# Kernel tuning notes

Measured on AMD Instinct MI355X. Metric: run time of the kernel, lower is better.

## Reference

```python
import jax, jax.numpy as jnp
import numpy as np

B = 2048
LF = 64
N_DEC, N_MOV, N_CAT, N_PER, N_COM = 12, 60000, 32, 100000, 20000


def setup_inputs() -> dict:
    key = jax.random.key(0)
    ks = jax.random.split(key, 10)

    def multihot(k, n):
        return jax.random.randint(k, (B, n), 0, 2, dtype=jnp.int32)

    def weight(k, n):
        # nn.Linear(n, LF, bias=False) weight, stored transposed as [n, LF]
        return jax.random.normal(k, (n, LF), dtype=jnp.float32) * 0.02

    return {
        "decade_idxs": multihot(ks[0], N_DEC),
        "movie_idxs": multihot(ks[1], N_MOV),
        "category_idxs": multihot(ks[2], N_CAT),
        "person_idxs": multihot(ks[3], N_PER),
        "company_idxs": multihot(ks[4], N_COM),
        "W_dec": weight(ks[5], N_DEC),
        "W_mov": weight(ks[6], N_MOV),
        "W_cat": weight(ks[7], N_CAT),
        "W_per": weight(ks[8], N_PER),
        "W_com": weight(ks[9], N_COM),
    }


def _norm_rows(emb, s):
    # divide rows whose multi-hot sum s is nonzero (np.flatnonzero semantics)
    mask = s != 0
    safe = jnp.where(mask, s, jnp.ones_like(s))
    return jnp.where(mask[:, None], emb / safe[:, None], emb)


def reference(decade_idxs, movie_idxs, category_idxs, person_idxs, company_idxs,
              W_dec, W_mov, W_cat, W_per, W_com):
    d = decade_idxs.astype(jnp.float32)
    m = movie_idxs.astype(jnp.float32)
    c = category_idxs.astype(jnp.float32)
    p = person_idxs.astype(jnp.float32)
    q = company_idxs.astype(jnp.float32)

    decades = d @ W_dec            # [B, LF]
    decades = _norm_rows(decades, jnp.sum(d, axis=1))

    movies = m @ W_mov
    # BUG in original module (replicated faithfully): `decades` is normalized
    # AGAIN by the movie-row sums; `movies` is never normalized.
    decades = _norm_rows(decades, jnp.sum(m, axis=1))

    categories = _norm_rows(c @ W_cat, jnp.sum(c, axis=1))
    persons = _norm_rows(p @ W_per, jnp.sum(p, axis=1))
    companies = _norm_rows(q @ W_com, jnp.sum(q, axis=1))

    return jnp.concatenate([decades, movies, categories, persons, companies], axis=1)
```

## Files before the change

kernel.cpp:

```cpp
#include <hip/hip_runtime.h>
#include <hip/hip_bf16.h>

#define LF 64
#define NBAGS 5
#define BROWS 2048
#define OUTC 320
#define KC 2048
#define MT_BLOCK 128
#define NMT (BROWS / MT_BLOCK)
#define NCHUNKS 90

#define WS_HEAD 65536
#define ZP_OFF 49152
#define WP_BYTES 23068672ull
#define PART_OFF (WS_HEAD + WP_BYTES)
#define PART_BYTES ((size_t)NCHUNKS * BROWS * LF * 4)

typedef __attribute__((ext_vector_type(8))) short short8;
typedef __attribute__((ext_vector_type(4))) float f32x4;

typedef const __attribute__((address_space(1))) void gas_t;
typedef __attribute__((address_space(3))) void las_t;

struct BagArgs {
    const int*   A[NBAGS];
    const float* W[NBAGS];
    int K[NBAGS];
    int cstart[NBAGS + 1];
    int tstart[NBAGS + 1];
};

__device__ __forceinline__ unsigned short f2bf(float f) {
    unsigned u = __float_as_uint(f);
    u += 0x7FFFu + ((u >> 16) & 1u);
    return (unsigned short)(u >> 16);
}

__global__ __launch_bounds__(256) void pack_w(BagArgs args,
                                              unsigned short* __restrict__ Wp) {
    __shared__ unsigned short ls[4][4096];
    const int wv = threadIdx.x >> 6;
    const int c  = threadIdx.x & 63;
    const int gtile = blockIdx.x * 4 + wv;

    int bag = 0;
#pragma unroll
    for (int b = 1; b < NBAGS; ++b)
        if (gtile >= args.tstart[b]) bag = b;
    const int lt = gtile - args.tstart[bag];
    const float* __restrict__ W = args.W[bag];
    const int K = args.K[bag];

    unsigned short* L = ls[wv];
#pragma unroll 8
    for (int k = 0; k < 64; ++k) {
        const int gk = lt * 64 + k;
        float v = (gk < K) ? W[(size_t)gk * LF + c] : 0.f;
        const int block = ((k >> 3) & 1) * 4 + (k >> 4);
        L[(block * LF + c) * 8 + (k & 7)] = f2bf(v);
    }
    __syncthreads();
    unsigned short* dst = Wp + ((size_t)gtile << 12);
#pragma unroll
    for (int j = 0; j < 8; ++j)
        *(short8*)(dst + c * 8 + j * 512) = *(const short8*)(L + c * 8 + j * 512);
}

__global__ __launch_bounds__(256) void bag_gemm(BagArgs args,
                                                const unsigned short* __restrict__ Wp,
                                                const int* __restrict__ zp,
                                                float* __restrict__ part,
                                                int* __restrict__ sums)
{
    __shared__ char lds[2][40960];

    const int tid  = threadIdx.x;
    const int wave = tid >> 6;
    const int lane = tid & 63;
    const int fr   = lane & 15;
    const int kg   = lane >> 4;

    const int g  = blockIdx.x >> 4;
    const int mt = blockIdx.x & 15;

    int bag = 1;
#pragma unroll
    for (int b = 2; b < NBAGS; ++b)
        if (g >= args.cstart[b]) bag = b;
    const int chunk  = g - args.cstart[bag];
    const int K      = args.K[bag];
    const int kc0    = chunk * KC;
    const int kend   = min(kc0 + KC, K);
    const int nsuper = (kend - kc0 + 63) >> 6;
    const int tile0  = args.tstart[bag] + chunk * (KC / 64);

    const int row0 = mt * MT_BLOCK + wave * 32;
    const int* __restrict__ Abase = args.A[bag];

    auto stage = [&](int ss, int bufi) {
        char* dA = &lds[bufi][0] + wave * 8192;
#pragma unroll
        for (int i = 0; i < 8; ++i) {
            const int rs = i & 1, j = i >> 1;
            const int col = kc0 + ss * 64 + kg * 16 + j * 4;
            const int row = row0 + rs * 16 + fr;
            const int* src = Abase + (size_t)row * K + col;
            if (col >= kend) src = zp;
            __builtin_amdgcn_global_load_lds((gas_t*)src, (las_t*)(dA + i * 1024),
                                             16, 0, 0);
        }
        const char* sB = (const char*)Wp + ((size_t)(tile0 + ss) << 13)
                         + wave * 2048 + lane * 16;
        char* dB = &lds[bufi][32768] + wave * 2048;
        __builtin_amdgcn_global_load_lds((gas_t*)sB, (las_t*)dB, 16, 0, 0);
        __builtin_amdgcn_global_load_lds((gas_t*)(sB + 1024), (las_t*)(dB + 1024),
                                         16, 0, 0);
    };

    f32x4 acc0[4], acc1[4];
#pragma unroll
    for (int i = 0; i < 4; ++i) {
        acc0[i] = (f32x4){0.f, 0.f, 0.f, 0.f};
        acc1[i] = (f32x4){0.f, 0.f, 0.f, 0.f};
    }
    int ps0 = 0, ps1 = 0;

    stage(0, 0);
    if (nsuper > 1) stage(1, 1);

    for (int ss = 0; ss < nsuper; ++ss) {
        const int cur = ss & 1;
        if (ss + 1 < nsuper) asm volatile("s_waitcnt vmcnt(10)" ::: "memory");
        else                 asm volatile("s_waitcnt vmcnt(0)"  ::: "memory");
        __builtin_amdgcn_sched_barrier(0);
        __builtin_amdgcn_s_barrier();

        const char* Ab = &lds[cur][0]     + wave * 8192 + kg * 256 + fr * 16;
        const char* Bb = &lds[cur][32768] + kg * 1024 + fr * 16;

        short8 fa[2][2];
#pragma unroll
        for (int m = 0; m < 2; ++m)
#pragma unroll
            for (int rs = 0; rs < 2; ++rs) {
                int4 lo = *(const int4*)(Ab + (size_t)(4 * m + rs) * 1024);
                int4 hi = *(const int4*)(Ab + (size_t)(4 * m + 2 + rs) * 1024);
                const int s = lo.x + lo.y + lo.z + lo.w + hi.x + hi.y + hi.z + hi.w;
                if (rs == 0) ps0 += s; else ps1 += s;
                const unsigned q0 = (unsigned)(lo.x | (lo.y << 16)) * 0x3F80u;
                const unsigned q1 = (unsigned)(lo.z | (lo.w << 16)) * 0x3F80u;
                const unsigned q2 = (unsigned)(hi.x | (hi.y << 16)) * 0x3F80u;
                const unsigned q3 = (unsigned)(hi.z | (hi.w << 16)) * 0x3F80u;
                int4 u = make_int4((int)q0, (int)q1, (int)q2, (int)q3);
                fa[rs][m] = *(short8*)&u;
            }
#pragma unroll
        for (int m = 0; m < 2; ++m)
#pragma unroll
            for (int ni = 0; ni < 4; ++ni) {
                const short8 y = *(const short8*)(Bb + m * 4096 + ni * 256);
                acc0[ni] = __builtin_amdgcn_mfma_f32_16x16x32_bf16(fa[0][m], y, acc0[ni], 0, 0, 0);
                acc1[ni] = __builtin_amdgcn_mfma_f32_16x16x32_bf16(fa[1][m], y, acc1[ni], 0, 0, 0);
            }

        __builtin_amdgcn_s_barrier();
        if (ss + 2 < nsuper) stage(ss + 2, cur);
    }

    ps0 += __shfl_xor(ps0, 16);
    ps0 += __shfl_xor(ps0, 32);
    ps1 += __shfl_xor(ps1, 16);
    ps1 += __shfl_xor(ps1, 32);
    if (kg == 0) {
        atomicAdd(&sums[bag * BROWS + row0 + fr], ps0);
        atomicAdd(&sums[bag * BROWS + row0 + 16 + fr], ps1);
    }

    float* dst = part + ((size_t)g * BROWS + row0 + kg * 4) * LF + fr;
#pragma unroll
    for (int ni = 0; ni < 4; ++ni)
#pragma unroll
        for (int r = 0; r < 4; ++r) {
            dst[(size_t)(r) * LF + ni * 16]      = acc0[ni][r];
            dst[(size_t)(16 + r) * LF + ni * 16] = acc1[ni][r];
        }
}

__global__ __launch_bounds__(256) void reduce_norm(BagArgs args,
                                                   const float* __restrict__ part,
                                                   float* __restrict__ out,
                                                   const int* __restrict__ sums)
{
    const int idx = blockIdx.x * 256 + threadIdx.x;
    if (idx >= BROWS * OUTC) return;
    const int row = idx / OUTC;
    const int c   = idx - row * OUTC;
    const int bag = c >> 6;
    const int col = c & 63;

    float v;
    if (bag == 0) {
        const int*   A0 = args.A[0];
        const float* W0 = args.W[0];
        float a = 0.f; int s = 0;
#pragma unroll
        for (int k = 0; k < 12; ++k) {
            const int x = A0[row * 12 + k];
            s += x;
            if (x) a += W0[k * LF + col];
        }
        if (s) a /= (float)s;
        const int sm = sums[1 * BROWS + row];
        if (sm) a /= (float)sm;
        v = a;
    } else {
        float a = 0.f;
        for (int gg = args.cstart[bag]; gg < args.cstart[bag + 1]; ++gg)
            a += part[((size_t)gg * BROWS + row) * LF + col];
        v = a;
        if (bag >= 2) {
            const int s = sums[bag * BROWS + row];
            if (s) v /= (float)s;
        }
    }
    out[idx] = v;
}

__global__ void naive_bag(BagArgs args, float* __restrict__ out) {
    const int row = blockIdx.x;
    const int c   = threadIdx.x;
    if (c >= OUTC) return;
    const int bag = c >> 6;
    const int col = c & 63;
    const int K = args.K[bag];
    const int* A = args.A[bag] + (size_t)row * K;
    const float* W = args.W[bag];
    float a = 0.f; int s = 0;
    for (int k = 0; k < K; ++k) {
        const int x = A[k];
        s += x;
        if (x) a += W[(size_t)k * LF + col];
    }
    if (bag != 1 && s) a /= (float)s;
    if (bag == 0) {
        const int* A1 = args.A[1] + (size_t)row * args.K[1];
        int sm = 0;
        for (int k = 0; k < args.K[1]; ++k) sm += A1[k];
        if (sm) a /= (float)sm;
    }
    out[(size_t)row * OUTC + c] = a;
}

extern "C" void kernel_launch(void* const* d_in, const int* in_sizes, int n_in,
                              void* d_out, int out_size, void* d_ws, size_t ws_size,
                              hipStream_t stream) {
    float* out = (float*)d_out;
    int* sums = (int*)d_ws;
    const int* zp = (const int*)((const char*)d_ws + ZP_OFF);
    unsigned short* Wp = (unsigned short*)((char*)d_ws + WS_HEAD);
    float* part = (float*)((char*)d_ws + PART_OFF);

    BagArgs args;
    const int Ks[NBAGS] = {12, 60000, 32, 100000, 20000};
    int tcum = 0;
    for (int b = 0; b < NBAGS; ++b) {
        args.A[b] = (const int*)d_in[b];
        args.W[b] = (const float*)d_in[5 + b];
        args.K[b] = Ks[b];
        args.tstart[b] = tcum;
        tcum += (Ks[b] + 63) / 64;
    }
    args.tstart[NBAGS] = tcum;
    args.cstart[0] = 0;
    int ccum = 0;
    for (int b = 1; b < NBAGS; ++b) {
        args.cstart[b] = ccum;
        ccum += (Ks[b] + KC - 1) / KC;
    }
    args.cstart[NBAGS] = ccum;

    const bool ok = ws_size >= PART_OFF + PART_BYTES;
    if (!ok) {
        naive_bag<<<BROWS, OUTC, 0, stream>>>(args, out);
        return;
    }

    hipMemsetAsync(d_ws, 0, WS_HEAD, stream);

    pack_w<<<tcum / 4, 256, 0, stream>>>(args, Wp);
    bag_gemm<<<NCHUNKS * NMT, 256, 0, stream>>>(args, Wp, zp, part, sums);
    reduce_norm<<<(BROWS * OUTC + 255) / 256, 256, 0, stream>>>(args, part, out, sums);
}
```

Baseline: 458.5 us.

## Compress multi-hot inputs to bitmaps before GEMM and drop LDS staging

Adds a compress kernel that reads the int32 multi-hot matrices once, packs them into bitmaps and computes the row sums. The GEMM then reads these bitmaps plus the packed weights straight into registers with two-stage register double buffering, replacing LDS staging and barriers, and expands bits into bf16 fragments. The aim is to cut repeated global traffic on the int32 inputs in the GEMM and remove synchronisation overhead. It adds a full extra pass over the inputs and a separate kernel launch, so the total bytes read may not drop much.

Result: slower. 560.8 us (+22.3%).

```diff
diff --git a/kernel.cpp b/kernel.cpp
--- a/kernel.cpp
+++ b/kernel.cpp
@@ -6,21 +6,20 @@
 #define BROWS 2048
 #define OUTC 320
 #define KC 2048
-#define MT_BLOCK 128
-#define NMT (BROWS / MT_BLOCK)
+#define NMT 16
 #define NCHUNKS 90
+#define NSLOTS 178
 
 #define WS_HEAD 65536
-#define ZP_OFF 49152
 #define WP_BYTES 23068672ull
-#define PART_OFF (WS_HEAD + WP_BYTES)
+#define BM_OFF (WS_HEAD + WP_BYTES)
+#define BM_BYTES 46661632ull
+#define PART_OFF (BM_OFF + BM_BYTES)
 #define PART_BYTES ((size_t)NCHUNKS * BROWS * LF * 4)
 
 typedef __attribute__((ext_vector_type(8))) short short8;
 typedef __attribute__((ext_vector_type(4))) float f32x4;
-
-typedef const __attribute__((address_space(1))) void gas_t;
-typedef __attribute__((address_space(3))) void las_t;
+typedef unsigned long long u64;
 
 struct BagArgs {
     const int*   A[NBAGS];
@@ -28,6 +27,8 @@
     int K[NBAGS];
     int cstart[NBAGS + 1];
     int tstart[NBAGS + 1];
+    int bmoff[NBAGS];
+    int rs[NBAGS];
 };
 
 __device__ __forceinline__ unsigned short f2bf(float f) {
@@ -66,14 +67,56 @@
         *(short8*)(dst + c * 8 + j * 512) = *(const short8*)(L + c * 8 + j * 512);
 }
 
+__global__ __launch_bounds__(256) void compress(BagArgs args,
+                                                unsigned char* __restrict__ bm,
+                                                int* __restrict__ sums) {
+    const int wv = threadIdx.x >> 6;
+    const int lane = threadIdx.x & 63;
+    const int slot = blockIdx.x * 4 + wv;
+    if (slot >= NSLOTS) return;
+    int bag, s0;
+    if      (slot >= 158) { bag = 4; s0 = 158; }
+    else if (slot >=  60) { bag = 3; s0 = 60;  }
+    else if (slot >=  59) { bag = 2; s0 = 59;  }
+    else                  { bag = 1; s0 = 0;   }
+    const int w   = slot - s0;
+    const int row = blockIdx.y;
+    const int K   = args.K[bag];
+    const int kb  = w * 1024;
+    const int* __restrict__ A = args.A[bag] + (size_t)row * K;
+    unsigned char* __restrict__ dst =
+        bm + args.bmoff[bag] + (size_t)row * args.rs[bag] + w * 128;
+
+    int cnt = 0;
+#pragma unroll
+    for (int s = 0; s < 4; ++s) {
+        const int k = kb + s * 256 + lane * 4;
+        int4 v = make_int4(0, 0, 0, 0);
+        if (k < K) v = *(const int4*)(A + k);
+        cnt += v.x + v.y + v.z + v.w;
+        const unsigned nib = (unsigned)(v.x | (v.y << 1) | (v.z << 2) | (v.w << 3));
+        u64 u = (u64)nib << ((lane & 15) * 4);
+        u |= __shfl_xor(u, 1);
+        u |= __shfl_xor(u, 2);
+        u |= __shfl_xor(u, 4);
+        u |= __shfl_xor(u, 8);
+        if ((lane & 15) == 0)
+            *(u64*)(dst + s * 32 + (lane >> 4) * 8) = u;
+    }
+    cnt += __shfl_xor(cnt, 1);
+    cnt += __shfl_xor(cnt, 2);
+    cnt += __shfl_xor(cnt, 4);
+    cnt += __shfl_xor(cnt, 8);
+    cnt += __shfl_xor(cnt, 16);
+    cnt += __shfl_xor(cnt, 32);
+    if (lane == 0) atomicAdd(&sums[bag * BROWS + row], cnt);
+}
+
 __global__ __launch_bounds__(256) void bag_gemm(BagArgs args,
                                                 const unsigned short* __restrict__ Wp,
-                                                const int* __restrict__ zp,
-                                                float* __restrict__ part,
-                                                int* __restrict__ sums)
+                                                const unsigned char* __restrict__ bm,
+                                                float* __restrict__ part)
 {
-    __shared__ char lds[2][40960];
-
     const int tid  = threadIdx.x;
     const int wave = tid >> 6;
     const int lane = tid & 63;
@@ -90,32 +133,15 @@
     const int chunk  = g - args.cstart[bag];
     const int K      = args.K[bag];
     const int kc0    = chunk * KC;
-    const int kend   = min(kc0 + KC, K);
-    const int nsuper = (kend - kc0 + 63) >> 6;
-    const int tile0  = args.tstart[bag] + chunk * (KC / 64);
-
-    const int row0 = mt * MT_BLOCK + wave * 32;
-    const int* __restrict__ Abase = args.A[bag];
-
-    auto stage = [&](int ss, int bufi) {
-        char* dA = &lds[bufi][0] + wave * 8192;
-#pragma unroll
-        for (int i = 0; i < 8; ++i) {
-            const int rs = i & 1, j = i >> 1;
-            const int col = kc0 + ss * 64 + kg * 16 + j * 4;
-            const int row = row0 + rs * 16 + fr;
-            const int* src = Abase + (size_t)row * K + col;
-            if (col >= kend) src = zp;
-            __builtin_amdgcn_global_load_lds((gas_t*)src, (las_t*)(dA + i * 1024),
-                                             16, 0, 0);
-        }
-        const char* sB = (const char*)Wp + ((size_t)(tile0 + ss) << 13)
-                         + wave * 2048 + lane * 16;
-        char* dB = &lds[bufi][32768] + wave * 2048;
-        __builtin_amdgcn_global_load_lds((gas_t*)sB, (las_t*)dB, 16, 0, 0);
-        __builtin_amdgcn_global_load_lds((gas_t*)(sB + 1024), (las_t*)(dB + 1024),
-                                         16, 0, 0);
-    };
+    const int ksz    = min(kc0 + KC, K) - kc0;
+    const int nsuper = (ksz + 63) >> 6;
+
+    const int row0 = mt * 128 + wave * 32;
+    const unsigned char* __restrict__ pb0 =
+        bm + args.bmoff[bag] + (size_t)(row0 + fr) * args.rs[bag] + (kc0 >> 3);
+    const unsigned char* __restrict__ pb1 = pb0 + (size_t)16 * args.rs[bag];
+    const unsigned short* __restrict__ pB =
+        Wp + ((size_t)(args.tstart[bag] + chunk * (KC / 64)) << 12) + (kg * LF + fr) * 8;
 
     f32x4 acc0[4], acc1[4];
 #pragma unroll
@@ -123,57 +149,61 @@
         acc0[i] = (f32x4){0.f, 0.f, 0.f, 0.f};
         acc1[i] = (f32x4){0.f, 0.f, 0.f, 0.f};
     }
-    int ps0 = 0, ps1 = 0;
-
-    stage(0, 0);
-    if (nsuper > 1) stage(1, 1);
-
-    for (int ss = 0; ss < nsuper; ++ss) {
-        const int cur = ss & 1;
-        if (ss + 1 < nsuper) asm volatile("s_waitcnt vmcnt(10)" ::: "memory");
-        else                 asm volatile("s_waitcnt vmcnt(0)"  ::: "memory");
+
+    auto loadA = [&](int ss, u64& x0, u64& x1) {
+        x0 = *(const u64*)(pb0 + ss * 8);
+        x1 = *(const u64*)(pb1 + ss * 8);
+    };
+    auto loadB = [&](int ss, short8 (&y)[2][4]) {
+        const unsigned short* p = pB + (size_t)ss * 4096;
+#pragma unroll
+        for (int m = 0; m < 2; ++m)
+#pragma unroll
+            for (int ni = 0; ni < 4; ++ni)
+                y[m][ni] = *(const short8*)(p + m * 2048 + ni * 128);
+    };
+
+    auto bf16pair = [](unsigned b) -> int {
+        return (int)((b & 1u) * 0x3F80u + (b & 2u) * 0x1FC00000u);
+    };
+    auto mkfrag = [&](unsigned byte) -> short8 {
+        int4 u = make_int4(bf16pair(byte), bf16pair(byte >> 2),
+                           bf16pair(byte >> 4), bf16pair(byte >> 6));
+        return *(short8*)&u;
+    };
+    auto compute = [&](u64 x0, u64 x1, const short8 (&y)[2][4]) {
+        const unsigned lo0 = (unsigned)(x0 >> (kg * 16));
+        const unsigned lo1 = (unsigned)(x1 >> (kg * 16));
+#pragma unroll
+        for (int m = 0; m < 2; ++m) {
+            const short8 fa0 = mkfrag((lo0 >> (m * 8)) & 0xFFu);
+            const short8 fa1 = mkfrag((lo1 >> (m * 8)) & 0xFFu);
+#pragma unroll
+            for (int ni = 0; ni < 4; ++ni) {
+                acc0[ni] = __builtin_amdgcn_mfma_f32_16x16x32_bf16(fa0, y[m][ni], acc0[ni], 0, 0, 0);
+                acc1[ni] = __builtin_amdgcn_mfma_f32_16x16x32_bf16(fa1, y[m][ni], acc1[ni], 0, 0, 0);
+            }
+        }
+    };
+
+    u64 Aa0, Aa1, Ab0, Ab1;
+    short8 Ba[2][4], Bb[2][4];
+    loadA(0, Aa0, Aa1);
+    loadB(0, Ba);
+    const int npair = (nsuper + 1) >> 1;
+    for (int p = 0; p < npair; ++p) {
+        const int s1  = 2 * p + 1;
+        const int s1c = min(s1, nsuper - 1);
+        loadA(s1c, Ab0, Ab1);
+        loadB(s1c, Bb);
         __builtin_amdgcn_sched_barrier(0);
-        __builtin_amdgcn_s_barrier();
-
-        const char* Ab = &lds[cur][0]     + wave * 8192 + kg * 256 + fr * 16;
-        const char* Bb = &lds[cur][32768] + kg * 1024 + fr * 16;
-
-        short8 fa[2][2];
-#pragma unroll
-        for (int m = 0; m < 2; ++m)
-#pragma unroll
-            for (int rs = 0; rs < 2; ++rs) {
-                int4 lo = *(const int4*)(Ab + (size_t)(4 * m + rs) * 1024);
-                int4 hi = *(const int4*)(Ab + (size_t)(4 * m + 2 + rs) * 1024);
-                const int s = lo.x + lo.y + lo.z + lo.w + hi.x + hi.y + hi.z + hi.w;
-                if (rs == 0) ps0 += s; else ps1 += s;
-                const unsigned q0 = (unsigned)(lo.x | (lo.y << 16)) * 0x3F80u;
-                const unsigned q1 = (unsigned)(lo.z | (lo.w << 16)) * 0x3F80u;
-                const unsigned q2 = (unsigned)(hi.x | (hi.y << 16)) * 0x3F80u;
-                const unsigned q3 = (unsigned)(hi.z | (hi.w << 16)) * 0x3F80u;
-                int4 u = make_int4((int)q0, (int)q1, (int)q2, (int)q3);
-                fa[rs][m] = *(short8*)&u;
-            }
-#pragma unroll
-        for (int m = 0; m < 2; ++m)
-#pragma unroll
-            for (int ni = 0; ni < 4; ++ni) {
-                const short8 y = *(const short8*)(Bb + m * 4096 + ni * 256);
-                acc0[ni] = __builtin_amdgcn_mfma_f32_16x16x32_bf16(fa[0][m], y, acc0[ni], 0, 0, 0);
-                acc1[ni] = __builtin_amdgcn_mfma_f32_16x16x32_bf16(fa[1][m], y, acc1[ni], 0, 0, 0);
-            }
-
-        __builtin_amdgcn_s_barrier();
-        if (ss + 2 < nsuper) stage(ss + 2, cur);
-    }
-
-    ps0 += __shfl_xor(ps0, 16);
-    ps0 += __shfl_xor(ps0, 32);
-    ps1 += __shfl_xor(ps1, 16);
-    ps1 += __shfl_xor(ps1, 32);
-    if (kg == 0) {
-        atomicAdd(&sums[bag * BROWS + row0 + fr], ps0);
-        atomicAdd(&sums[bag * BROWS + row0 + 16 + fr], ps1);
+        compute(Aa0, Aa1, Ba);
+        const int s2c = min(2 * p + 2, nsuper - 1);
+        loadA(s2c, Aa0, Aa1);
+        loadB(s2c, Ba);
+        __builtin_amdgcn_sched_barrier(0);
+        if (s1 < nsuper)
+            compute(Ab0, Ab1, Bb);
     }
 
     float* dst = part + ((size_t)g * BROWS + row0 + kg * 4) * LF + fr;
@@ -256,8 +286,8 @@
                               hipStream_t stream) {
     float* out = (float*)d_out;
     int* sums = (int*)d_ws;
-    const int* zp = (const int*)((const char*)d_ws + ZP_OFF);
     unsigned short* Wp = (unsigned short*)((char*)d_ws + WS_HEAD);
+    unsigned char* bm  = (unsigned char*)((char*)d_ws + BM_OFF);
     float* part = (float*)((char*)d_ws + PART_OFF);
 
     BagArgs args;
@@ -279,15 +309,25 @@
     }
     args.cstart[NBAGS] = ccum;
 
+    args.rs[0] = 0;
+    int bcum = 0;
+    for (int b = 1; b < NBAGS; ++b) {
+        args.rs[b] = ((Ks[b] + 1023) / 1024) * 128;
+        args.bmoff[b] = bcum;
+        bcum += BROWS * args.rs[b];
+    }
+    args.bmoff[0] = 0;
+
     const bool ok = ws_size >= PART_OFF + PART_BYTES;
     if (!ok) {
         naive_bag<<<BROWS, OUTC, 0, stream>>>(args, out);
         return;
     }
 
-    hipMemsetAsync(d_ws, 0, WS_HEAD, stream);
+    hipMemsetAsync(sums, 0, NBAGS * BROWS * sizeof(int), stream);
 
     pack_w<<<tcum / 4, 256, 0, stream>>>(args, Wp);
-    bag_gemm<<<NCHUNKS * NMT, 256, 0, stream>>>(args, Wp, zp, part, sums);
+    compress<<<dim3((NSLOTS + 3) / 4, BROWS), 256, 0, stream>>>(args, bm, sums);
+    bag_gemm<<<NCHUNKS * NMT, 256, 0, stream>>>(args, Wp, bm, part);
     reduce_norm<<<(BROWS * OUTC + 255) / 256, 256, 0, stream>>>(args, part, out, sums);
 }
```

## Bit-pack multi-hot rows in LDS, halve K chunk, compute row sums via MFMA

Applied to the files above, without the earlier changes.

The GEMM kernel now loads each 128x1024 block of int32 multi-hot data straight into registers and packs it into a 1-bit-per-element bitmap in LDS (XOR-swizzled), replacing the double-buffered global_load_lds staging of full int32 tiles. B fragments are read directly from global memory, and A fragments are rebuilt from the bitmap bits. Row sums come from an extra MFMA against an all-ones vector and are accumulated as floats, replacing the integer reductions. KC halves to 1024 so there are twice as many chunks and partial buffers, and launch bounds ask for 4 blocks per CU. The A load is no longer pipelined against compute, and the reduce pass has to read more partials.

Result: slower. 579.3 us (+26.4%).

```diff
diff --git a/kernel.cpp b/kernel.cpp
--- a/kernel.cpp
+++ b/kernel.cpp
@@ -5,22 +5,18 @@
 #define NBAGS 5
 #define BROWS 2048
 #define OUTC 320
-#define KC 2048
-#define MT_BLOCK 128
-#define NMT (BROWS / MT_BLOCK)
-#define NCHUNKS 90
+#define KC 1024
+#define NMT 16
+#define NCHUNKS 178
 
 #define WS_HEAD 65536
-#define ZP_OFF 49152
-#define WP_BYTES 23068672ull
+#define NTILES 2864
+#define WP_BYTES ((size_t)NTILES * 8192)
 #define PART_OFF (WS_HEAD + WP_BYTES)
 #define PART_BYTES ((size_t)NCHUNKS * BROWS * LF * 4)
 
 typedef __attribute__((ext_vector_type(8))) short short8;
 typedef __attribute__((ext_vector_type(4))) float f32x4;
-
-typedef const __attribute__((address_space(1))) void gas_t;
-typedef __attribute__((address_space(3))) void las_t;
 
 struct BagArgs {
     const int*   A[NBAGS];
@@ -66,13 +62,12 @@
         *(short8*)(dst + c * 8 + j * 512) = *(const short8*)(L + c * 8 + j * 512);
 }
 
-__global__ __launch_bounds__(256) void bag_gemm(BagArgs args,
-                                                const unsigned short* __restrict__ Wp,
-                                                const int* __restrict__ zp,
-                                                float* __restrict__ part,
-                                                int* __restrict__ sums)
+__global__ __launch_bounds__(256, 4) void bag_gemm(BagArgs args,
+                                                   const unsigned short* __restrict__ Wp,
+                                                   float* __restrict__ part,
+                                                   float* __restrict__ sums)
 {
-    __shared__ char lds[2][40960];
+    __shared__ unsigned bits[128 * 32];
 
     const int tid  = threadIdx.x;
     const int wave = tid >> 6;
@@ -87,35 +82,42 @@
 #pragma unroll
     for (int b = 2; b < NBAGS; ++b)
         if (g >= args.cstart[b]) bag = b;
-    const int chunk  = g - args.cstart[bag];
-    const int K      = args.K[bag];
-    const int kc0    = chunk * KC;
-    const int kend   = min(kc0 + KC, K);
-    const int nsuper = (kend - kc0 + 63) >> 6;
-    const int tile0  = args.tstart[bag] + chunk * (KC / 64);
-
-    const int row0 = mt * MT_BLOCK + wave * 32;
+    const int chunk = g - args.cstart[bag];
+    const int K     = args.K[bag];
+    const int kc0   = chunk * KC;
+    const int row0b = mt * 128;
+    const int row0w = wave * 32;
     const int* __restrict__ Abase = args.A[bag];
 
-    auto stage = [&](int ss, int bufi) {
-        char* dA = &lds[bufi][0] + wave * 8192;
-#pragma unroll
-        for (int i = 0; i < 8; ++i) {
-            const int rs = i & 1, j = i >> 1;
-            const int col = kc0 + ss * 64 + kg * 16 + j * 4;
-            const int row = row0 + rs * 16 + fr;
-            const int* src = Abase + (size_t)row * K + col;
-            if (col >= kend) src = zp;
-            __builtin_amdgcn_global_load_lds((gas_t*)src, (las_t*)(dA + i * 1024),
-                                             16, 0, 0);
-        }
-        const char* sB = (const char*)Wp + ((size_t)(tile0 + ss) << 13)
-                         + wave * 2048 + lane * 16;
-        char* dB = &lds[bufi][32768] + wave * 2048;
-        __builtin_amdgcn_global_load_lds((gas_t*)sB, (las_t*)dB, 16, 0, 0);
-        __builtin_amdgcn_global_load_lds((gas_t*)(sB + 1024), (las_t*)(dB + 1024),
-                                         16, 0, 0);
-    };
+    for (int it = 0; it < 16; ++it) {
+        const int rr = row0w + it * 2;
+        int4 v[8];
+#pragma unroll
+        for (int q = 0; q < 8; ++q) {
+            const int row = row0b + rr + (q >> 2);
+            const int col = kc0 + (q & 3) * 256 + lane * 4;
+            const int* p = Abase + (size_t)row * K + min(col, K - 4);
+            const int4 z = make_int4(0, 0, 0, 0);
+            v[q] = (col < K) ? *(const int4*)p : z;
+        }
+#pragma unroll
+        for (int q = 0; q < 8; ++q) {
+            unsigned u = (unsigned)(v[q].x | (v[q].y << 1) | (v[q].z << 2) | (v[q].w << 3))
+                         << ((lane & 7) * 4);
+            u |= __shfl_xor(u, 1);
+            u |= __shfl_xor(u, 2);
+            u |= __shfl_xor(u, 4);
+            if ((lane & 7) == 0) {
+                const int row = rr + (q >> 2);
+                const int w   = (q & 3) * 8 + (lane >> 3);
+                bits[row * 32 + (w ^ (row & 31))] = u;
+            }
+        }
+    }
+    __syncthreads();
+
+    const unsigned short* __restrict__ pB =
+        Wp + ((size_t)(args.tstart[bag] + chunk * 16) << 12) + (kg * LF + fr) * 8;
 
     f32x4 acc0[4], acc1[4];
 #pragma unroll
@@ -123,60 +125,57 @@
         acc0[i] = (f32x4){0.f, 0.f, 0.f, 0.f};
         acc1[i] = (f32x4){0.f, 0.f, 0.f, 0.f};
     }
-    int ps0 = 0, ps1 = 0;
-
-    stage(0, 0);
-    if (nsuper > 1) stage(1, 1);
-
-    for (int ss = 0; ss < nsuper; ++ss) {
-        const int cur = ss & 1;
-        if (ss + 1 < nsuper) asm volatile("s_waitcnt vmcnt(10)" ::: "memory");
-        else                 asm volatile("s_waitcnt vmcnt(0)"  ::: "memory");
-        __builtin_amdgcn_sched_barrier(0);
-        __builtin_amdgcn_s_barrier();
-
-        const char* Ab = &lds[cur][0]     + wave * 8192 + kg * 256 + fr * 16;
-        const char* Bb = &lds[cur][32768] + kg * 1024 + fr * 16;
-
-        short8 fa[2][2];
+    f32x4 accS0 = (f32x4){0.f, 0.f, 0.f, 0.f};
+    f32x4 accS1 = (f32x4){0.f, 0.f, 0.f, 0.f};
+    const int4 uo = make_int4(0x3F803F80, 0x3F803F80, 0x3F803F80, 0x3F803F80);
+    const short8 ones = *(const short8*)&uo;
+
+    auto bf16pair = [](unsigned b) -> int {
+        return (int)((b & 1u) * 0x3F80u + (b & 2u) * 0x1FC00000u);
+    };
+    auto mkfrag = [&](unsigned byte) -> short8 {
+        int4 u = make_int4(bf16pair(byte), bf16pair(byte >> 2),
+                           bf16pair(byte >> 4), bf16pair(byte >> 6));
+        return *(short8*)&u;
+    };
+
+    for (int ss = 0; ss < 16; ++ss) {
+        const unsigned short* p = pB + (size_t)ss * 4096;
+        short8 y[2][4];
 #pragma unroll
         for (int m = 0; m < 2; ++m)
 #pragma unroll
-            for (int rs = 0; rs < 2; ++rs) {
-                int4 lo = *(const int4*)(Ab + (size_t)(4 * m + rs) * 1024);
-                int4 hi = *(const int4*)(Ab + (size_t)(4 * m + 2 + rs) * 1024);
-                const int s = lo.x + lo.y + lo.z + lo.w + hi.x + hi.y + hi.z + hi.w;
-                if (rs == 0) ps0 += s; else ps1 += s;
-                const unsigned q0 = (unsigned)(lo.x | (lo.y << 16)) * 0x3F80u;
-                const unsigned q1 = (unsigned)(lo.z | (lo.w << 16)) * 0x3F80u;
-                const unsigned q2 = (unsigned)(hi.x | (hi.y << 16)) * 0x3F80u;
-                const unsigned q3 = (unsigned)(hi.z | (hi.w << 16)) * 0x3F80u;
-                int4 u = make_int4((int)q0, (int)q1, (int)q2, (int)q3);
-                fa[rs][m] = *(short8*)&u;
+            for (int ni = 0; ni < 4; ++ni)
+                y[m][ni] = *(const short8*)(p + m * 2048 + ni * 128);
+
+        const int wi = 2 * ss + (kg >> 1);
+        const unsigned wrd0 = bits[(row0w + fr) * 32 + (wi ^ fr)];
+        const unsigned wrd1 = bits[(row0w + 16 + fr) * 32 + (wi ^ (fr + 16))];
+
+#pragma unroll
+        for (int m = 0; m < 2; ++m) {
+            const int sh = (kg & 1) * 16 + m * 8;
+            const short8 fa0 = mkfrag((wrd0 >> sh) & 0xFFu);
+            const short8 fa1 = mkfrag((wrd1 >> sh) & 0xFFu);
+            accS0 = __builtin_amdgcn_mfma_f32_16x16x32_bf16(fa0, ones, accS0, 0, 0, 0);
+            accS1 = __builtin_amdgcn_mfma_f32_16x16x32_bf16(fa1, ones, accS1, 0, 0, 0);
+#pragma unroll
+            for (int ni = 0; ni < 4; ++ni) {
+                acc0[ni] = __builtin_amdgcn_mfma_f32_16x16x32_bf16(fa0, y[m][ni], acc0[ni], 0, 0, 0);
+                acc1[ni] = __builtin_amdgcn_mfma_f32_16x16x32_bf16(fa1, y[m][ni], acc1[ni], 0, 0, 0);
             }
-#pragma unroll
-        for (int m = 0; m < 2; ++m)
-#pragma unroll
-            for (int ni = 0; ni < 4; ++ni) {
-                const short8 y = *(const short8*)(Bb + m * 4096 + ni * 256);
-                acc0[ni] = __builtin_amdgcn_mfma_f32_16x16x32_bf16(fa[0][m], y, acc0[ni], 0, 0, 0);
-                acc1[ni] = __builtin_amdgcn_mfma_f32_16x16x32_bf16(fa[1][m], y, acc1[ni], 0, 0, 0);
-            }
-
-        __builtin_amdgcn_s_barrier();
-        if (ss + 2 < nsuper) stage(ss + 2, cur);
-    }
-
-    ps0 += __shfl_xor(ps0, 16);
-    ps0 += __shfl_xor(ps0, 32);
-    ps1 += __shfl_xor(ps1, 16);
-    ps1 += __shfl_xor(ps1, 32);
-    if (kg == 0) {
-        atomicAdd(&sums[bag * BROWS + row0 + fr], ps0);
-        atomicAdd(&sums[bag * BROWS + row0 + 16 + fr], ps1);
-    }
-
-    float* dst = part + ((size_t)g * BROWS + row0 + kg * 4) * LF + fr;
+        }
+    }
+
+    if (fr == 0) {
+#pragma unroll
+        for (int r = 0; r < 4; ++r) {
+            atomicAdd(&sums[bag * BROWS + row0b + row0w + kg * 4 + r],      accS0[r]);
+            atomicAdd(&sums[bag * BROWS + row0b + row0w + 16 + kg * 4 + r], accS1[r]);
+        }
+    }
+
+    float* dst = part + ((size_t)g * BROWS + row0b + row0w + kg * 4) * LF + fr;
 #pragma unroll
     for (int ni = 0; ni < 4; ++ni)
 #pragma unroll
@@ -189,7 +188,7 @@
 __global__ __launch_bounds__(256) void reduce_norm(BagArgs args,
                                                    const float* __restrict__ part,
                                                    float* __restrict__ out,
-                                                   const int* __restrict__ sums)
+                                                   const float* __restrict__ sums)
 {
     const int idx = blockIdx.x * 256 + threadIdx.x;
     if (idx >= BROWS * OUTC) return;
@@ -210,8 +209,8 @@
             if (x) a += W0[k * LF + col];
         }
         if (s) a /= (float)s;
-        const int sm = sums[1 * BROWS + row];
-        if (sm) a /= (float)sm;
+        const float sm = sums[1 * BROWS + row];
+        if (sm != 0.f) a /= sm;
         v = a;
     } else {
         float a = 0.f;
@@ -219,8 +218,8 @@
             a += part[((size_t)gg * BROWS + row) * LF + col];
         v = a;
         if (bag >= 2) {
-            const int s = sums[bag * BROWS + row];
-            if (s) v /= (float)s;
+            const float s = sums[bag * BROWS + row];
+            if (s != 0.f) v /= s;
         }
     }
     out[idx] = v;
@@ -255,8 +254,7 @@
                               void* d_out, int out_size, void* d_ws, size_t ws_size,
                               hipStream_t stream) {
     float* out = (float*)d_out;
-    int* sums = (int*)d_ws;
-    const int* zp = (const int*)((const char*)d_ws + ZP_OFF);
+    float* sums = (float*)d_ws;
     unsigned short* Wp = (unsigned short*)((char*)d_ws + WS_HEAD);
     float* part = (float*)((char*)d_ws + PART_OFF);
 
@@ -268,7 +266,7 @@
         args.W[b] = (const float*)d_in[5 + b];
         args.K[b] = Ks[b];
         args.tstart[b] = tcum;
-        tcum += (Ks[b] + 63) / 64;
+        tcum += ((Ks[b] + KC - 1) / KC) * 16;
     }
     args.tstart[NBAGS] = tcum;
     args.cstart[0] = 0;
@@ -285,9 +283,9 @@
         return;
     }
 
-    hipMemsetAsync(d_ws, 0, WS_HEAD, stream);
+    hipMemsetAsync(sums, 0, NBAGS * BROWS * sizeof(float), stream);
 
     pack_w<<<tcum / 4, 256, 0, stream>>>(args, Wp);
-    bag_gemm<<<NCHUNKS * NMT, 256, 0, stream>>>(args, Wp, zp, part, sums);
+    bag_gemm<<<NCHUNKS * NMT, 256, 0, stream>>>(args, Wp, part, sums);
     reduce_norm<<<(BROWS * OUTC + 255) / 256, 256, 0, stream>>>(args, part, out, sums);
 }
```
